# Optimization experiments

Measured on AMD Instinct MI355X. Metric: run time of the kernel, lower is better.

## Reference

```python
import jax, jax.numpy as jnp
import numpy as np
from math import factorial, sqrt

# (mul, l) lists after e3nn normalization/mul-splitting (muls already aligned)
RS1 = [(256, 0), (256, 1), (256, 2)]
RS2 = [(256, 1), (256, 1), (256, 2)]


def _su2_cg(j1, m1, j2, m2, j3, m3):
    # Racah formula for SU(2) Clebsch-Gordan <j1 m1 j2 m2 | j3 m3> (e3nn convention)
    if m3 != m1 + m2:
        return 0.0
    vmin = max(-j1 + j2 + m3, -j1 + m1, 0)
    vmax = min(j2 + j3 + m1, j3 - j1 + j2, j3 + m3)
    f = factorial
    C = sqrt((2 * j3 + 1)
             * f(j3 + j1 - j2) * f(j3 - j1 + j2) * f(j1 + j2 - j3) * f(j3 + m3) * f(j3 - m3)
             / (f(j1 + j2 + j3 + 1) * f(j1 - m1) * f(j1 + m1) * f(j2 - m2) * f(j2 + m2)))
    S = 0.0
    for v in range(vmin, vmax + 1):
        S += (-1.0) ** (v + j2 + m2) * (f(j2 + j3 + m1 - v) * f(j1 - m1 + v)
             / (f(v) * f(j3 - j1 + j2 - v) * f(j3 + m3 - v) * f(v + j1 - j2 - m3)))
    return C * S


def _su2_cg_tensor(j1, j2, j3):
    mat = np.zeros((2 * j1 + 1, 2 * j2 + 1, 2 * j3 + 1))
    for m1 in range(-j1, j1 + 1):
        for m2 in range(-j2, j2 + 1):
            m3 = m1 + m2
            if abs(m3) <= j3:
                mat[j1 + m1, j2 + m2, j3 + m3] = _su2_cg(j1, m1, j2, m2, j3, m3)
    return mat / sqrt(2 * j3 + 1)  # Wigner-3j normalization


def _q(l):
    # change of basis real -> complex spherical harmonics (e3nn convention)
    q = np.zeros((2 * l + 1, 2 * l + 1), dtype=np.complex128)
    for m in range(-l, 0):
        q[l + m, l + abs(m)] = 1.0 / sqrt(2)
        q[l + m, l - abs(m)] = -1j / sqrt(2)
    q[l, l] = 1.0
    for m in range(1, l + 1):
        q[l + m, l + abs(m)] = (-1) ** m / sqrt(2)
        q[l + m, l - abs(m)] = 1j * (-1) ** m / sqrt(2)
    return (-1j) ** l * q


def _wigner3j(l1, l2, l3):
    # real-basis Wigner 3j tensor, shape (2l1+1, 2l2+1, 2l3+1)
    C = _su2_cg_tensor(l1, l2, l3)
    Q1, Q2, Q3 = _q(l1), _q(l2), _q(l3)
    C = np.einsum('ij,kl,nm,ikn->jlm', Q1, Q2, np.conj(Q3), C)
    assert np.abs(C.imag).max() < 1e-6
    return C.real


# precomputed CG blocks C[(l, l1, l2)] of shape (2l+1, 2l1+1, 2l2+1), scaled by sqrt(2l+1)
CG = {}
for (_mul1, _l1), (_mul2, _l2) in zip(RS1, RS2):
    if _l1 != 0 and _l2 != 0:
        for _l in range(abs(_l1 - _l2), _l1 + _l2 + 1):
            CG[(_l, _l1, _l2)] = jnp.asarray(_wigner3j(_l, _l1, _l2) * sqrt(2 * _l + 1), dtype=jnp.float32)


def _forward(features_1, features_2):
    size = features_1.shape[:-1]
    f1 = features_1.reshape(-1, features_1.shape[-1])
    f2 = features_2.reshape(-1, features_2.shape[-1])
    B = f1.shape[0]
    out, i1, i2 = [], 0, 0
    for (mul, l1), (_, l2) in zip(RS1, RS2):
        d1, d2 = 2 * l1 + 1, 2 * l2 + 1
        x1 = f1[:, i1:i1 + mul * d1].reshape(B, mul, d1)
        i1 += mul * d1
        x2 = f2[:, i2:i2 + mul * d2].reshape(B, mul, d2)
        i2 += mul * d2
        if l1 == 0 or l2 == 0:
            # CG with a scalar is (a multiple of) identity -> elementwise product
            out.append((x1 * x2).reshape(B, -1))
        else:
            for l in range(abs(l1 - l2), l1 + l2 + 1):
                C = CG[(l, l1, l2)]  # (2l+1, d1, d2)
                out.append(jnp.einsum('ijk,bmj,bmk->bmi', C, x1, x2).reshape(B, -1))
    return jnp.concatenate(out, axis=1).reshape(*size, -1)


def setup_inputs() -> dict:
    key = jax.random.key(0)
    k1, k2 = jax.random.split(key)
    n1 = sum(m * (2 * l + 1) for m, l in RS1)  # 2304
    n2 = sum(m * (2 * l + 1) for m, l in RS2)  # 2816
    B = 8192
    return {
        'features_1': jax.random.normal(k1, (B, n1), dtype=jnp.float32),
        'features_2': jax.random.normal(k2, (B, n2), dtype=jnp.float32),
    }


def reference(features_1, features_2):
    return _forward(features_1, features_2)
```

## Files before the change

### kernel.cpp

```cpp
#include <hip/hip_runtime.h>

namespace cg {

constexpr double fact(int n) {
  double r = 1.0;
  for (int i = 2; i <= n; ++i) r *= (double)i;
  return r;
}

constexpr double csqrt(double x) {
  if (x <= 0.0) return 0.0;
  double g = x < 1.0 ? 1.0 : x;
  for (int i = 0; i < 80; ++i) g = 0.5 * (g + x / g);
  return g;
}

struct cplx { double re, im; };
constexpr cplx cmul(cplx a, cplx b) {
  return cplx{a.re * b.re - a.im * b.im, a.re * b.im + a.im * b.re};
}

constexpr double su2_cg(int j1, int m1, int j2, int m2, int j3, int m3) {
  if (m3 != m1 + m2) return 0.0;
  int vmin = -j1 + j2 + m3;
  if (-j1 + m1 > vmin) vmin = -j1 + m1;
  if (0 > vmin) vmin = 0;
  int vmax = j2 + j3 + m1;
  if (j3 - j1 + j2 < vmax) vmax = j3 - j1 + j2;
  if (j3 + m3 < vmax) vmax = j3 + m3;
  const double C = csqrt((2.0 * j3 + 1.0)
      * fact(j3 + j1 - j2) * fact(j3 - j1 + j2) * fact(j1 + j2 - j3)
      * fact(j3 + m3) * fact(j3 - m3)
      / (fact(j1 + j2 + j3 + 1) * fact(j1 - m1) * fact(j1 + m1)
         * fact(j2 - m2) * fact(j2 + m2)));
  double S = 0.0;
  for (int v = vmin; v <= vmax; ++v) {
    const double sgn = ((v + j2 + m2) & 1) ? -1.0 : 1.0;
    S += sgn * (fact(j2 + j3 + m1 - v) * fact(j1 - m1 + v)
         / (fact(v) * fact(j3 - j1 + j2 - v) * fact(j3 + m3 - v)
            * fact(v + j1 - j2 - m3)));
  }
  return C * S;
}

template <int L> struct QMat { cplx q[2 * L + 1][2 * L + 1]; };

template <int L>
constexpr QMat<L> make_q() {
  QMat<L> Q{};
  const double s = 1.0 / csqrt(2.0);
  for (int m = -L; m < 0; ++m) {
    Q.q[L + m][L - m] = cplx{s, 0.0};
    Q.q[L + m][L + m] = cplx{0.0, -s};
  }
  Q.q[L][L] = cplx{1.0, 0.0};
  for (int m = 1; m <= L; ++m) {
    const double sg = (m & 1) ? -1.0 : 1.0;
    Q.q[L + m][L + m] = cplx{sg * s, 0.0};
    Q.q[L + m][L - m] = cplx{0.0, sg * s};
  }
  cplx p{1.0, 0.0};
  for (int t = 0; t < L; ++t) p = cmul(p, cplx{0.0, -1.0});
  for (int r = 0; r < 2 * L + 1; ++r)
    for (int c = 0; c < 2 * L + 1; ++c)
      Q.q[r][c] = cmul(p, Q.q[r][c]);
  return Q;
}

template <int L, int L1, int L2>
struct W3 { float t[2 * L + 1][2 * L1 + 1][2 * L2 + 1]; };

template <int L, int L1, int L2>
constexpr W3<L, L1, L2> wigner() {
  const QMat<L>  Q1 = make_q<L>();
  const QMat<L1> Q2 = make_q<L1>();
  const QMat<L2> Q3 = make_q<L2>();
  double C[2 * L + 1][2 * L1 + 1][2 * L2 + 1] = {};
  for (int m1 = -L; m1 <= L; ++m1)
    for (int m2 = -L1; m2 <= L1; ++m2) {
      const int m3 = m1 + m2;
      if (m3 >= -L2 && m3 <= L2)
        C[L + m1][L1 + m2][L2 + m3] = su2_cg(L, m1, L1, m2, L2, m3);
    }
  const double scale = csqrt(2.0 * L + 1.0) / csqrt(2.0 * L2 + 1.0);
  W3<L, L1, L2> R{};
  for (int j = 0; j < 2 * L + 1; ++j)
    for (int l = 0; l < 2 * L1 + 1; ++l)
      for (int m = 0; m < 2 * L2 + 1; ++m) {
        cplx acc{0.0, 0.0};
        for (int i = 0; i < 2 * L + 1; ++i) {
          const cplx q1 = Q1.q[i][j];
          if (q1.re == 0.0 && q1.im == 0.0) continue;
          for (int k = 0; k < 2 * L1 + 1; ++k) {
            const cplx q2 = Q2.q[k][l];
            if (q2.re == 0.0 && q2.im == 0.0) continue;
            const cplx q12 = cmul(q1, q2);
            for (int n = 0; n < 2 * L2 + 1; ++n) {
              const double c = C[i][k][n];
              if (c == 0.0) continue;
              const cplx q3c{Q3.q[n][m].re, -Q3.q[n][m].im};
              const cplx term = cmul(q12, q3c);
              acc.re += term.re * c;
              acc.im += term.im * c;
            }
          }
        }
        R.t[j][l][m] = (float)(acc.re * scale);
      }
  return R;
}

constexpr W3<0, 1, 1> W011 = wigner<0, 1, 1>();
constexpr W3<1, 1, 1> W111 = wigner<1, 1, 1>();
constexpr W3<2, 1, 1> W211 = wigner<2, 1, 1>();
constexpr W3<0, 2, 2> W022 = wigner<0, 2, 2>();
constexpr W3<1, 2, 2> W122 = wigner<1, 2, 2>();
constexpr W3<2, 2, 2> W222 = wigner<2, 2, 2>();
constexpr W3<3, 2, 2> W322 = wigner<3, 2, 2>();
constexpr W3<4, 2, 2> W422 = wigner<4, 2, 2>();

}


template <int L, int L1, int L2>
__device__ __forceinline__ void contract(const cg::W3<L, L1, L2>& W,
                                         const float (&p)[2 * L1 + 1][2 * L2 + 1],
                                         float* __restrict__ o) {
#pragma unroll
  for (int i = 0; i < 2 * L + 1; ++i) {
    float acc = 0.0f;
#pragma unroll
    for (int j = 0; j < 2 * L1 + 1; ++j)
#pragma unroll
      for (int k = 0; k < 2 * L2 + 1; ++k) {
        const float c = W.t[i][j][k];
        if (c != 0.0f) acc = __builtin_fmaf(c, p[j][k], acc);
      }
    o[i] = acc;
  }
}

__global__ __launch_bounds__(256) void tp_kernel(
    const float* __restrict__ f1, const float* __restrict__ f2,
    float* __restrict__ out, int B) {
  __shared__ __align__(16) float lds[9472];
  const int b = blockIdx.x;
  if (b >= B) return;
  const int m = threadIdx.x;
  const float* F1 = f1 + (size_t)b * 2304;
  const float* F2 = f2 + (size_t)b * 2816;

  const float s0 = F1[m];
  float a1[3], a2[5], ca[3], cb[3], cc[5];
#pragma unroll
  for (int j = 0; j < 3; ++j) a1[j] = F1[256 + m * 3 + j];
#pragma unroll
  for (int j = 0; j < 5; ++j) a2[j] = F1[1024 + m * 5 + j];
#pragma unroll
  for (int k = 0; k < 3; ++k) ca[k] = F2[m * 3 + k];
#pragma unroll
  for (int k = 0; k < 3; ++k) cb[k] = F2[768 + m * 3 + k];
#pragma unroll
  for (int k = 0; k < 5; ++k) cc[k] = F2[1536 + m * 5 + k];

  float r0[3];
#pragma unroll
  for (int k = 0; k < 3; ++k) r0[k] = s0 * ca[k];

  float o0, o1[3], o2[5];
  {
    float p[3][3];
#pragma unroll
    for (int j = 0; j < 3; ++j)
#pragma unroll
      for (int k = 0; k < 3; ++k) p[j][k] = a1[j] * cb[k];
    contract<0, 1, 1>(cg::W011, p, &o0);
    contract<1, 1, 1>(cg::W111, p, o1);
    contract<2, 1, 1>(cg::W211, p, o2);
  }
  float q0, q1[3], q2[5], q3[7], q4[9];
  {
    float p[5][5];
#pragma unroll
    for (int j = 0; j < 5; ++j)
#pragma unroll
      for (int k = 0; k < 5; ++k) p[j][k] = a2[j] * cc[k];
    contract<0, 2, 2>(cg::W022, p, &q0);
    contract<1, 2, 2>(cg::W122, p, q1);
    contract<2, 2, 2>(cg::W222, p, q2);
    contract<3, 2, 2>(cg::W322, p, q3);
    contract<4, 2, 2>(cg::W422, p, q4);
  }

#pragma unroll
  for (int k = 0; k < 3; ++k) lds[m * 3 + k] = r0[k];
  lds[768 + m] = o0;
#pragma unroll
  for (int i = 0; i < 3; ++i) lds[1024 + m * 3 + i] = o1[i];
#pragma unroll
  for (int i = 0; i < 5; ++i) lds[1792 + m * 5 + i] = o2[i];
  lds[3072 + m] = q0;
#pragma unroll
  for (int i = 0; i < 3; ++i) lds[3328 + m * 3 + i] = q1[i];
#pragma unroll
  for (int i = 0; i < 5; ++i) lds[4096 + m * 5 + i] = q2[i];
#pragma unroll
  for (int i = 0; i < 7; ++i) lds[5376 + m * 7 + i] = q3[i];
#pragma unroll
  for (int i = 0; i < 9; ++i) lds[7168 + m * 9 + i] = q4[i];
  __syncthreads();

  {
    const float4* l4 = reinterpret_cast<const float4*>(lds);
    float4* dst = reinterpret_cast<float4*>(out + (size_t)b * 9472);
#pragma unroll
    for (int k = 0; k < 9; ++k) dst[m + k * 256] = l4[m + k * 256];
    if (m < 64) dst[2304 + m] = l4[2304 + m];
  }
}

extern "C" void kernel_launch(void* const* d_in, const int* in_sizes, int n_in,
                              void* d_out, int out_size, void* d_ws, size_t ws_size,
                              hipStream_t stream) {
  const float* f1 = (const float*)d_in[0];
  const float* f2 = (const float*)d_in[1];
  float* out = (float*)d_out;
  const int B = in_sizes[0] / 2304;
  tp_kernel<<<B, 256, 0, stream>>>(f1, f2, out, B);
}
```

Measured before the change: 92.74 us.

## Use per-wavefront LDS staging without block barrier and nontemporal loads/stores

Each 64-lane wavefront now stages its own slice of every output segment in a private LDS region and writes that slice to global memory itself, so the block-wide __syncthreads is replaced by a compiler memory fence. Input loads and output stores become nontemporal to avoid polluting the caches with streaming data. Removing the barrier lets wavefronts proceed independently. The trade-offs are irregular store predicates, with some lanes idle on partial segments, and reliance on wavefront-synchronous LDS visibility without an explicit barrier.

```diff
diff --git a/kernel.cpp b/kernel.cpp
--- a/kernel.cpp
+++ b/kernel.cpp
@@ -122,6 +122,8 @@
 }
 
 
+typedef float f32x4 __attribute__((ext_vector_type(4)));
+
 template <int L, int L1, int L2>
 __device__ __forceinline__ void contract(const cg::W3<L, L1, L2>& W,
                                          const float (&p)[2 * L1 + 1][2 * L2 + 1],
@@ -146,22 +148,26 @@
   __shared__ __align__(16) float lds[9472];
   const int b = blockIdx.x;
   if (b >= B) return;
-  const int m = threadIdx.x;
+  const int w = threadIdx.x >> 6;
+  const int l = threadIdx.x & 63;
+  const int m = 64 * w + l;
+  float* Wr = lds + w * 2368;
+
   const float* F1 = f1 + (size_t)b * 2304;
   const float* F2 = f2 + (size_t)b * 2816;
 
-  const float s0 = F1[m];
+  const float s0 = __builtin_nontemporal_load(&F1[m]);
   float a1[3], a2[5], ca[3], cb[3], cc[5];
 #pragma unroll
-  for (int j = 0; j < 3; ++j) a1[j] = F1[256 + m * 3 + j];
-#pragma unroll
-  for (int j = 0; j < 5; ++j) a2[j] = F1[1024 + m * 5 + j];
-#pragma unroll
-  for (int k = 0; k < 3; ++k) ca[k] = F2[m * 3 + k];
-#pragma unroll
-  for (int k = 0; k < 3; ++k) cb[k] = F2[768 + m * 3 + k];
-#pragma unroll
-  for (int k = 0; k < 5; ++k) cc[k] = F2[1536 + m * 5 + k];
+  for (int j = 0; j < 3; ++j) a1[j] = __builtin_nontemporal_load(&F1[256 + m * 3 + j]);
+#pragma unroll
+  for (int j = 0; j < 5; ++j) a2[j] = __builtin_nontemporal_load(&F1[1024 + m * 5 + j]);
+#pragma unroll
+  for (int k = 0; k < 3; ++k) ca[k] = __builtin_nontemporal_load(&F2[m * 3 + k]);
+#pragma unroll
+  for (int k = 0; k < 3; ++k) cb[k] = __builtin_nontemporal_load(&F2[768 + m * 3 + k]);
+#pragma unroll
+  for (int k = 0; k < 5; ++k) cc[k] = __builtin_nontemporal_load(&F2[1536 + m * 5 + k]);
 
   float r0[3];
 #pragma unroll
@@ -193,29 +199,41 @@
   }
 
 #pragma unroll
-  for (int k = 0; k < 3; ++k) lds[m * 3 + k] = r0[k];
-  lds[768 + m] = o0;
-#pragma unroll
-  for (int i = 0; i < 3; ++i) lds[1024 + m * 3 + i] = o1[i];
-#pragma unroll
-  for (int i = 0; i < 5; ++i) lds[1792 + m * 5 + i] = o2[i];
-  lds[3072 + m] = q0;
-#pragma unroll
-  for (int i = 0; i < 3; ++i) lds[3328 + m * 3 + i] = q1[i];
-#pragma unroll
-  for (int i = 0; i < 5; ++i) lds[4096 + m * 5 + i] = q2[i];
-#pragma unroll
-  for (int i = 0; i < 7; ++i) lds[5376 + m * 7 + i] = q3[i];
-#pragma unroll
-  for (int i = 0; i < 9; ++i) lds[7168 + m * 9 + i] = q4[i];
-  __syncthreads();
+  for (int k = 0; k < 3; ++k) Wr[l * 3 + k] = r0[k];
+  Wr[192 + l] = o0;
+#pragma unroll
+  for (int k = 0; k < 3; ++k) Wr[256 + l * 3 + k] = o1[k];
+#pragma unroll
+  for (int k = 0; k < 5; ++k) Wr[448 + l * 5 + k] = o2[k];
+  Wr[768 + l] = q0;
+#pragma unroll
+  for (int k = 0; k < 3; ++k) Wr[832 + l * 3 + k] = q1[k];
+#pragma unroll
+  for (int k = 0; k < 5; ++k) Wr[1024 + l * 5 + k] = q2[k];
+#pragma unroll
+  for (int k = 0; k < 7; ++k) Wr[1344 + l * 7 + k] = q3[k];
+#pragma unroll
+  for (int k = 0; k < 9; ++k) Wr[1792 + l * 9 + k] = q4[k];
+
+  asm volatile("" ::: "memory");
 
   {
-    const float4* l4 = reinterpret_cast<const float4*>(lds);
-    float4* dst = reinterpret_cast<float4*>(out + (size_t)b * 9472);
-#pragma unroll
-    for (int k = 0; k < 9; ++k) dst[m + k * 256] = l4[m + k * 256];
-    if (m < 64) dst[2304 + m] = l4[2304 + m];
+    const f32x4* OF = reinterpret_cast<const f32x4*>(Wr);
+    f32x4* D = reinterpret_cast<f32x4*>(out + (size_t)b * 9472);
+    if (l < 48) __builtin_nontemporal_store(OF[l], &D[48 * w + l]);
+    if (l < 16) __builtin_nontemporal_store(OF[48 + l], &D[192 + 16 * w + l]);
+    if (l < 48) __builtin_nontemporal_store(OF[64 + l], &D[256 + 48 * w + l]);
+    __builtin_nontemporal_store(OF[112 + l], &D[448 + 80 * w + l]);
+    if (l < 16) __builtin_nontemporal_store(OF[176 + l], &D[448 + 80 * w + 64 + l]);
+    if (l < 16) __builtin_nontemporal_store(OF[192 + l], &D[768 + 16 * w + l]);
+    if (l < 48) __builtin_nontemporal_store(OF[208 + l], &D[832 + 48 * w + l]);
+    __builtin_nontemporal_store(OF[256 + l], &D[1024 + 80 * w + l]);
+    if (l < 16) __builtin_nontemporal_store(OF[320 + l], &D[1024 + 80 * w + 64 + l]);
+    __builtin_nontemporal_store(OF[336 + l], &D[1344 + 112 * w + l]);
+    if (l < 48) __builtin_nontemporal_store(OF[400 + l], &D[1344 + 112 * w + 64 + l]);
+    __builtin_nontemporal_store(OF[448 + l], &D[1792 + 144 * w + l]);
+    __builtin_nontemporal_store(OF[512 + l], &D[1792 + 144 * w + 64 + l]);
+    if (l < 16) __builtin_nontemporal_store(OF[576 + l], &D[1792 + 144 * w + 128 + l]);
   }
 }
 
```

New measurement: 86.15 us. 7.1% less time.
